# Performance work log

Hardware: AMD Instinct MI355X
Metric: run time of the kernel (lower is better)

Reference implementation:

```python
import jax, jax.numpy as jnp
import numpy as np

N_NODES = 100000
N_EDGES = 640000
IN_DIM = 64
HID = 128
NUM_GRAPHS = 128
MPNN_STEPS = 3
S2S_STEPS = 3


def setup_inputs() -> dict:
    key = jax.random.key(0)
    ks = jax.random.split(key, 20)
    x = jax.random.normal(ks[0], (N_NODES, IN_DIM), dtype=jnp.float32)
    edge_index = jax.random.randint(ks[1], (2, N_EDGES), 0, N_NODES, dtype=jnp.int32)
    batch = jnp.sort(jax.random.randint(ks[2], (N_NODES,), 0, NUM_GRAPHS, dtype=jnp.int32))
    s = 1.0 / np.sqrt(HID)
    params = {
        # input layer Linear(64 -> 128)
        'W_in': jax.random.normal(ks[3], (HID, IN_DIM), dtype=jnp.float32) * s,
        'b_in': jax.random.normal(ks[4], (HID,), dtype=jnp.float32) * s,
        # MGU parameters (torch.randn init in source)
        'W_f': jax.random.normal(ks[5], (HID, HID), dtype=jnp.float32),
        'U_f': jax.random.normal(ks[6], (HID, HID), dtype=jnp.float32),
        'b_f': jax.random.normal(ks[7], (HID,), dtype=jnp.float32),
        'W_h': jax.random.normal(ks[8], (HID, HID), dtype=jnp.float32),
        'U_h': jax.random.normal(ks[9], (HID, HID), dtype=jnp.float32),
        'b_h': jax.random.normal(ks[10], (HID,), dtype=jnp.float32),
        # Set2Set LSTM: input 2*HID, hidden HID, gate order i,f,g,o
        'lstm_w_ih': jax.random.normal(ks[11], (4 * HID, 2 * HID), dtype=jnp.float32) * s,
        'lstm_w_hh': jax.random.normal(ks[12], (4 * HID, HID), dtype=jnp.float32) * s,
        'lstm_b_ih': jax.random.normal(ks[13], (4 * HID,), dtype=jnp.float32) * s,
        'lstm_b_hh': jax.random.normal(ks[14], (4 * HID,), dtype=jnp.float32) * s,
        # prediction layer Linear(2*HID -> 1)
        'W_pred': jax.random.normal(ks[15], (1, 2 * HID), dtype=jnp.float32) * s,
        'b_pred': jax.random.normal(ks[16], (1,), dtype=jnp.float32) * s,
    }
    return {'x': x, 'edge_index': edge_index, 'batch': batch, **params}


def _mpnn_mgu(h, src, dst, W_f, U_f, b_f, W_h, U_h, b_h):
    # sum-aggregate neighbor messages: m_i = sum_{j->i} h_j
    m = jax.ops.segment_sum(h[src], dst, num_segments=N_NODES)  # [N, H]
    f_t = jax.nn.sigmoid(m @ W_f.T + h @ U_f.T + b_f)
    h_hat = jnp.tanh(m @ W_h.T + (f_t * h) @ U_h.T + b_h)
    return (1.0 - f_t) * h + f_t * h_hat


def _set2set(x, batch, w_ih, w_hh, b_ih, b_hh):
    G, H = NUM_GRAPHS, HID
    q_star = jnp.zeros((G, 2 * H), dtype=x.dtype)
    h_l = jnp.zeros((G, H), dtype=x.dtype)
    c_l = jnp.zeros((G, H), dtype=x.dtype)
    for _ in range(S2S_STEPS):
        gates = q_star @ w_ih.T + h_l @ w_hh.T + b_ih + b_hh  # [G, 4H]
        i, f, g, o = jnp.split(gates, 4, axis=-1)
        c_l = jax.nn.sigmoid(f) * c_l + jax.nn.sigmoid(i) * jnp.tanh(g)
        h_l = jax.nn.sigmoid(o) * jnp.tanh(c_l)
        q = h_l  # [G, H]
        # attention over nodes within each graph segment
        e = jnp.sum(x * q[batch], axis=-1)  # [N]
        e_max = jax.ops.segment_max(e, batch, num_segments=G)
        a_un = jnp.exp(e - e_max[batch])
        denom = jax.ops.segment_sum(a_un, batch, num_segments=G)
        a = a_un / denom[batch]
        r = jax.ops.segment_sum(a[:, None] * x, batch, num_segments=G)  # [G, H]
        q_star = jnp.concatenate([q, r], axis=-1)
    return q_star


def reference(x, edge_index, batch, W_in, b_in, W_f, U_f, b_f, W_h, U_h, b_h,
              lstm_w_ih, lstm_w_hh, lstm_b_ih, lstm_b_hh, W_pred, b_pred):
    h = jax.nn.relu(x @ W_in.T + b_in)  # [N, HID]
    src, dst = edge_index[0], edge_index[1]
    for _ in range(MPNN_STEPS):
        h = _mpnn_mgu(h, src, dst, W_f, U_f, b_f, W_h, U_h, b_h)
    q_star = _set2set(h, batch, lstm_w_ih, lstm_w_hh, lstm_b_ih, lstm_b_hh)  # [G, 2H]
    return q_star @ W_pred.T + b_pred  # [G, 1]
```

## Files before the change

### kernel.cpp

```cpp
#include <hip/hip_runtime.h>
#include <math.h>

#define N_NODES 100000
#define N_EDGES 640000
#define IN_DIM 64
#define HID 128
#define NGRAPH 128

typedef __bf16 bf16x2 __attribute__((ext_vector_type(2)));
typedef __bf16 bf16x4 __attribute__((ext_vector_type(4)));
typedef __bf16 bf16x8 __attribute__((ext_vector_type(8)));
typedef float f32x4 __attribute__((ext_vector_type(4)));

#define LDST 136

__device__ __forceinline__ float sigmoid_f(float z) {
  return __fdividef(1.f, 1.f + __expf(-z));
}
__device__ __forceinline__ float tanh_f(float z) {
  return 1.f - __fdividef(2.f, __expf(2.f * z) + 1.f);
}

__device__ __forceinline__ void fma44(const float4 A[4], const float4 B[4], float acc[4][4]) {
#pragma unroll
  for (int i2 = 0; i2 < 4; ++i2) {
    acc[i2][0] += A[i2].x*B[0].x + A[i2].y*B[1].x + A[i2].z*B[2].x + A[i2].w*B[3].x;
    acc[i2][1] += A[i2].x*B[0].y + A[i2].y*B[1].y + A[i2].z*B[2].y + A[i2].w*B[3].y;
    acc[i2][2] += A[i2].x*B[0].z + A[i2].y*B[1].z + A[i2].z*B[2].z + A[i2].w*B[3].z;
    acc[i2][3] += A[i2].x*B[0].w + A[i2].y*B[1].w + A[i2].z*B[2].w + A[i2].w*B[3].w;
  }
}

__global__ __launch_bounds__(256) void k_input(const float* __restrict__ x,
                                               const float* __restrict__ W,
                                               const float* __restrict__ b,
                                               float* __restrict__ h) {
  __shared__ float wS[64][132];
  __shared__ float xS[32][68];
  int t = threadIdx.x;
  int nb = blockIdx.x * 32;
#pragma unroll
  for (int i = 0; i < 8; ++i) {
    int idx4 = i * 256 + t;
    int j = idx4 >> 4, kq = idx4 & 15;
    float4 v = ((const float4*)W)[j * 16 + kq];
    wS[4*kq+0][j] = v.x; wS[4*kq+1][j] = v.y; wS[4*kq+2][j] = v.z; wS[4*kq+3][j] = v.w;
  }
#pragma unroll
  for (int i = 0; i < 2; ++i) {
    int idx4 = i * 256 + t;
    int n = idx4 >> 4, kq = idx4 & 15;
    float4 v = ((const float4*)x)[(nb + n) * 16 + kq];
    *((float4*)&xS[n][4*kq]) = v;
  }
  __syncthreads();
  int bq = t & 31, a = t >> 5;
  float acc[4][4] = {};
#pragma unroll
  for (int kk4 = 0; kk4 < 16; ++kk4) {
    float4 A[4], B[4];
#pragma unroll
    for (int i2 = 0; i2 < 4; ++i2) A[i2] = *((const float4*)&xS[4*a+i2][4*kk4]);
#pragma unroll
    for (int c = 0; c < 4; ++c) B[c] = *((const float4*)&wS[4*kk4+c][4*bq]);
    fma44(A, B, acc);
  }
  float4 bb = ((const float4*)b)[bq];
  float ba[4] = {bb.x, bb.y, bb.z, bb.w};
#pragma unroll
  for (int i2 = 0; i2 < 4; ++i2) {
    float4 o;
    o.x = fmaxf(acc[i2][0] + ba[0], 0.f);
    o.y = fmaxf(acc[i2][1] + ba[1], 0.f);
    o.z = fmaxf(acc[i2][2] + ba[2], 0.f);
    o.w = fmaxf(acc[i2][3] + ba[3], 0.f);
    ((float4*)h)[(nb + 4*a + i2) * 32 + bq] = o;
  }
}

__global__ __launch_bounds__(256) void k_hist(const int* __restrict__ dst,
                                              int* __restrict__ deg) {
  int e = blockIdx.x * 256 + threadIdx.x;
  if (e < N_EDGES) atomicAdd(&deg[dst[e]], 1);
}

#define SCAN_CHUNK 4096
#define SCAN_NB 25

__global__ __launch_bounds__(256) void k_scan_part(const int* __restrict__ deg,
                                                   int* __restrict__ bsum) {
  __shared__ int red[256];
  int t = threadIdx.x, b = blockIdx.x;
  int base = b * SCAN_CHUNK + t * 16;
  int s = 0;
#pragma unroll
  for (int i = 0; i < 16; ++i) {
    int idx = base + i;
    if (idx < N_NODES) s += deg[idx];
  }
  red[t] = s;
  __syncthreads();
  for (int off = 128; off > 0; off >>= 1) {
    if (t < off) red[t] += red[t + off];
    __syncthreads();
  }
  if (t == 0) bsum[b] = red[0];
}

__global__ void k_scan_mid(const int* __restrict__ bsum, int* __restrict__ boff,
                           int* __restrict__ rowstart) {
  if (threadIdx.x == 0) {
    int run = 0;
    for (int i = 0; i < SCAN_NB; ++i) { boff[i] = run; run += bsum[i]; }
    rowstart[N_NODES] = run;
  }
}

__global__ __launch_bounds__(256) void k_scan_final(const int* __restrict__ deg,
                                                    const int* __restrict__ boff,
                                                    int* __restrict__ rowstart) {
  __shared__ int ts[256];
  int t = threadIdx.x, b = blockIdx.x;
  int base = b * SCAN_CHUNK + t * 16;
  int v[16];
  int s = 0;
#pragma unroll
  for (int i = 0; i < 16; ++i) {
    int idx = base + i;
    v[i] = (idx < N_NODES) ? deg[idx] : 0;
    s += v[i];
  }
  ts[t] = s;
  __syncthreads();
  for (int off = 1; off < 256; off <<= 1) {
    int add = (t >= off) ? ts[t - off] : 0;
    __syncthreads();
    ts[t] += add;
    __syncthreads();
  }
  int run = boff[b] + ts[t] - s;
#pragma unroll
  for (int i = 0; i < 16; ++i) {
    int idx = base + i;
    if (idx < N_NODES) rowstart[idx] = run;
    run += v[i];
  }
}

__global__ __launch_bounds__(256) void k_fill(const int* __restrict__ src,
                                              const int* __restrict__ dst,
                                              int* __restrict__ cursor,
                                              int* __restrict__ srcSorted) {
  int e = blockIdx.x * 256 + threadIdx.x;
  if (e >= N_EDGES) return;
  int d = dst[e];
  int p = atomicAdd(&cursor[d], 1);
  srcSorted[p] = src[e];
}

__global__ __launch_bounds__(256) void k_wsplit(const float* __restrict__ W0,
                                                const float* __restrict__ W1,
                                                const float* __restrict__ W2,
                                                const float* __restrict__ W3,
                                                __bf16* __restrict__ Whi,
                                                __bf16* __restrict__ Wlo) {
  int id = blockIdx.x * 256 + threadIdx.x;
  int mat = id >> 14, idx = id & 16383;
  const float* W = (mat == 0) ? W0 : (mat == 1) ? W1 : (mat == 2) ? W2 : W3;
  float v = W[idx];
  __bf16 hi = (__bf16)v;
  Whi[id] = hi;
  Wlo[id] = (__bf16)(v - (float)hi);
}

__global__ __launch_bounds__(256, 4) void k_mgu(float* __restrict__ hdst,
                                                const float* __restrict__ hsrc,
                                                const int* __restrict__ rowstart,
                                                const int* __restrict__ srcSorted,
                                                const __bf16* __restrict__ Whi,
                                                const __bf16* __restrict__ Wlo,
                                                const float* __restrict__ bfp,
                                                const float* __restrict__ bhp) {
  __shared__ __bf16 mHi[32 * LDST], mLo[32 * LDST];
  __shared__ __bf16 hHi[32 * LDST], hLo[32 * LDST];
  const int t = threadIdx.x;
  const int nb = blockIdx.x * 32;

#pragma unroll
  for (int i = 0; i < 4; ++i) {
    int idx4 = i * 256 + t;
    int n = idx4 >> 5, kq = idx4 & 31;
    float4 vh = ((const float4*)hsrc)[(nb + n) * 32 + kq];
    bf16x4 hh, hl;
    hh[0] = (__bf16)vh.x; hl[0] = (__bf16)(vh.x - (float)hh[0]);
    hh[1] = (__bf16)vh.y; hl[1] = (__bf16)(vh.y - (float)hh[1]);
    hh[2] = (__bf16)vh.z; hl[2] = (__bf16)(vh.z - (float)hh[2]);
    hh[3] = (__bf16)vh.w; hl[3] = (__bf16)(vh.w - (float)hh[3]);
    int e0 = n * LDST + 4 * kq;
    *(bf16x4*)&hHi[e0] = hh; *(bf16x4*)&hLo[e0] = hl;
  }

  {
    const int grp = t >> 5, li = t & 31;
    const float4* h4 = (const float4*)hsrc;
#pragma unroll
    for (int c = 0; c < 4; ++c) {
      int nl = c * 8 + grp;
      int node = nb + nl;
      int j0 = rowstart[node], j1 = rowstart[node + 1];
      float4 a0 = {0.f, 0.f, 0.f, 0.f}, a1 = {0.f, 0.f, 0.f, 0.f};
      float4 a2 = {0.f, 0.f, 0.f, 0.f}, a3 = {0.f, 0.f, 0.f, 0.f};
      int j = j0;
      for (; j + 3 < j1; j += 4) {
        int s0 = srcSorted[j], s1 = srcSorted[j + 1];
        int s2 = srcSorted[j + 2], s3 = srcSorted[j + 3];
        float4 v0 = h4[s0 * 32 + li];
        float4 v1 = h4[s1 * 32 + li];
        float4 v2 = h4[s2 * 32 + li];
        float4 v3 = h4[s3 * 32 + li];
        a0.x += v0.x; a0.y += v0.y; a0.z += v0.z; a0.w += v0.w;
        a1.x += v1.x; a1.y += v1.y; a1.z += v1.z; a1.w += v1.w;
        a2.x += v2.x; a2.y += v2.y; a2.z += v2.z; a2.w += v2.w;
        a3.x += v3.x; a3.y += v3.y; a3.z += v3.z; a3.w += v3.w;
      }
      if (j + 1 < j1) {
        int s0 = srcSorted[j], s1 = srcSorted[j + 1];
        float4 v0 = h4[s0 * 32 + li];
        float4 v1 = h4[s1 * 32 + li];
        a0.x += v0.x; a0.y += v0.y; a0.z += v0.z; a0.w += v0.w;
        a1.x += v1.x; a1.y += v1.y; a1.z += v1.z; a1.w += v1.w;
        j += 2;
      }
      if (j < j1) {
        int s0 = srcSorted[j];
        float4 v0 = h4[s0 * 32 + li];
        a0.x += v0.x; a0.y += v0.y; a0.z += v0.z; a0.w += v0.w;
      }
      float4 o = {a0.x + a1.x + a2.x + a3.x, a0.y + a1.y + a2.y + a3.y,
                  a0.z + a1.z + a2.z + a3.z, a0.w + a1.w + a2.w + a3.w};
      bf16x4 mh, ml;
      mh[0] = (__bf16)o.x; ml[0] = (__bf16)(o.x - (float)mh[0]);
      mh[1] = (__bf16)o.y; ml[1] = (__bf16)(o.y - (float)mh[1]);
      mh[2] = (__bf16)o.z; ml[2] = (__bf16)(o.z - (float)mh[2]);
      mh[3] = (__bf16)o.w; ml[3] = (__bf16)(o.w - (float)mh[3]);
      int e0 = nl * LDST + 4 * li;
      *(bf16x4*)&mHi[e0] = mh; *(bf16x4*)&mLo[e0] = ml;
    }
  }
  __syncthreads();

  const int w = t >> 6, l = t & 63;
  const int lj = l & 15, q = l >> 4;

  float bfj[2], bhj[2];
#pragma unroll
  for (int ct = 0; ct < 2; ++ct) {
    int j = (2 * w + ct) * 16 + lj;
    bfj[ct] = bfp[j];
    bhj[ct] = bhp[j];
  }

  f32x4 acc[2][2] = {};

#pragma unroll
  for (int kc = 0; kc < 128; kc += 32) {
    bf16x8 bwh[2], bwl[2], buh[2], bul[2];
#pragma unroll
    for (int ct = 0; ct < 2; ++ct) {
      int off = ((2 * w + ct) * 16 + lj) * 128 + kc + q * 8;
      bwh[ct] = *(const bf16x8*)&Whi[off];
      bwl[ct] = *(const bf16x8*)&Wlo[off];
      buh[ct] = *(const bf16x8*)&Whi[16384 + off];
      bul[ct] = *(const bf16x8*)&Wlo[16384 + off];
    }
#pragma unroll
    for (int rt = 0; rt < 2; ++rt) {
      int e0 = (rt * 16 + lj) * LDST + kc + q * 8;
      bf16x8 amh = *(const bf16x8*)&mHi[e0];
      bf16x8 aml = *(const bf16x8*)&mLo[e0];
      bf16x8 ahh = *(const bf16x8*)&hHi[e0];
      bf16x8 ahl = *(const bf16x8*)&hLo[e0];
#pragma unroll
      for (int ct = 0; ct < 2; ++ct) {
        f32x4 a = acc[rt][ct];
        a = __builtin_amdgcn_mfma_f32_16x16x32_bf16(amh, bwh[ct], a, 0, 0, 0);
        a = __builtin_amdgcn_mfma_f32_16x16x32_bf16(amh, bwl[ct], a, 0, 0, 0);
        a = __builtin_amdgcn_mfma_f32_16x16x32_bf16(aml, bwh[ct], a, 0, 0, 0);
        a = __builtin_amdgcn_mfma_f32_16x16x32_bf16(ahh, buh[ct], a, 0, 0, 0);
        a = __builtin_amdgcn_mfma_f32_16x16x32_bf16(ahh, bul[ct], a, 0, 0, 0);
        a = __builtin_amdgcn_mfma_f32_16x16x32_bf16(ahl, buh[ct], a, 0, 0, 0);
        acc[rt][ct] = a;
      }
    }
  }

  __syncthreads();
  float fv[2][2][4], hvv[2][2][4];
#pragma unroll
  for (int rt = 0; rt < 2; ++rt)
#pragma unroll
    for (int ct = 0; ct < 2; ++ct) {
      int j = (2 * w + ct) * 16 + lj;
#pragma unroll
      for (int r = 0; r < 4; ++r) {
        int nl = rt * 16 + q * 4 + r;
        float z = acc[rt][ct][r] + bfj[ct];
        float f = sigmoid_f(z);
        int he = nl * LDST + j;
        float hval = (float)hHi[he] + (float)hLo[he];
        float g = f * hval;
        __bf16 ghi = (__bf16)g;
        hHi[he] = ghi;
        hLo[he] = (__bf16)(g - (float)ghi);
        fv[rt][ct][r] = f;
        hvv[rt][ct][r] = hval;
        acc[rt][ct][r] = 0.f;
      }
    }
  __syncthreads();

#pragma unroll
  for (int kc = 0; kc < 128; kc += 32) {
    bf16x8 bwh[2], bwl[2], buh[2], bul[2];
#pragma unroll
    for (int ct = 0; ct < 2; ++ct) {
      int off = ((2 * w + ct) * 16 + lj) * 128 + kc + q * 8;
      bwh[ct] = *(const bf16x8*)&Whi[2 * 16384 + off];
      bwl[ct] = *(const bf16x8*)&Wlo[2 * 16384 + off];
      buh[ct] = *(const bf16x8*)&Whi[3 * 16384 + off];
      bul[ct] = *(const bf16x8*)&Wlo[3 * 16384 + off];
    }
#pragma unroll
    for (int rt = 0; rt < 2; ++rt) {
      int e0 = (rt * 16 + lj) * LDST + kc + q * 8;
      bf16x8 amh = *(const bf16x8*)&mHi[e0];
      bf16x8 aml = *(const bf16x8*)&mLo[e0];
      bf16x8 agh = *(const bf16x8*)&hHi[e0];
      bf16x8 agl = *(const bf16x8*)&hLo[e0];
#pragma unroll
      for (int ct = 0; ct < 2; ++ct) {
        f32x4 a = acc[rt][ct];
        a = __builtin_amdgcn_mfma_f32_16x16x32_bf16(amh, bwh[ct], a, 0, 0, 0);
        a = __builtin_amdgcn_mfma_f32_16x16x32_bf16(amh, bwl[ct], a, 0, 0, 0);
        a = __builtin_amdgcn_mfma_f32_16x16x32_bf16(aml, bwh[ct], a, 0, 0, 0);
        a = __builtin_amdgcn_mfma_f32_16x16x32_bf16(agh, buh[ct], a, 0, 0, 0);
        a = __builtin_amdgcn_mfma_f32_16x16x32_bf16(agh, bul[ct], a, 0, 0, 0);
        a = __builtin_amdgcn_mfma_f32_16x16x32_bf16(agl, buh[ct], a, 0, 0, 0);
        acc[rt][ct] = a;
      }
    }
  }

#pragma unroll
  for (int rt = 0; rt < 2; ++rt)
#pragma unroll
    for (int ct = 0; ct < 2; ++ct) {
      int j = (2 * w + ct) * 16 + lj;
#pragma unroll
      for (int r = 0; r < 4; ++r) {
        int node = nb + rt * 16 + q * 4 + r;
        float T = tanh_f(acc[rt][ct][r] + bhj[ct]);
        float f = fv[rt][ct][r];
        float hn = (1.f - f) * hvv[rt][ct][r] + f * T;
        hdst[node * 128 + j] = hn;
      }
    }
}

__global__ __launch_bounds__(1024) void k_s2s(const float* __restrict__ h,
                                              const int* __restrict__ batch,
                                              const float* __restrict__ w_ih,
                                              const float* __restrict__ w_hh,
                                              const float* __restrict__ b_ih,
                                              const float* __restrict__ b_hh,
                                              const float* __restrict__ Wp,
                                              const float* __restrict__ bp,
                                              float* __restrict__ out) {
  const int g = blockIdx.x, t = threadIdx.x;
  const int w = t >> 6, l = t & 63;
  const int half = l >> 5, li = l & 31;
  const int hw = 2 * w + half;
  __shared__ float qs[256];
  __shared__ float hl[128], cl[128];
  __shared__ float gates[512];
  __shared__ float redM[32], redS[32], scl[32];
  __shared__ float rPart[32][132];
  __shared__ float gInvS;
  __shared__ int bnd[2];

  if (t < 2) {
    int tgt = g + t;
    int lo = 0, hi = N_NODES;
    while (lo < hi) { int mid = (lo + hi) >> 1; if (batch[mid] < tgt) lo = mid + 1; else hi = mid; }
    bnd[t] = lo;
  }
  if (t < 256) qs[t] = 0.f;
  if (t < 128) { hl[t] = 0.f; cl[t] = 0.f; }
  __syncthreads();
  const int s0 = bnd[0], s1 = bnd[1];

  for (int step = 0; step < 3; ++step) {
#pragma unroll 2
    for (int jt = w; jt < 512; jt += 16) {
      const float* wi = w_ih + jt * 256;
      const float* wh = w_hh + jt * 128;
      float s = qs[l] * wi[l] + qs[l+64] * wi[l+64]
              + qs[l+128] * wi[l+128] + qs[l+192] * wi[l+192]
              + hl[l] * wh[l] + hl[l+64] * wh[l+64];
#pragma unroll
      for (int o = 32; o > 0; o >>= 1) s += __shfl_xor(s, o, 64);
      if (l == 0) gates[jt] = s + b_ih[jt] + b_hh[jt];
    }
    __syncthreads();
    if (t < 128) {
      float gi = gates[t], gf = gates[128 + t], gg = gates[256 + t], go = gates[384 + t];
      float c = sigmoid_f(gf) * cl[t] + sigmoid_f(gi) * tanh_f(gg);
      float hh = sigmoid_f(go) * tanh_f(c);
      cl[t] = c;
      hl[t] = hh;
      qs[t] = hh;
    }
    __syncthreads();

    float mw = -INFINITY, sw = 0.f;
    float4 racc = {0.f, 0.f, 0.f, 0.f};
    const float4* h4 = (const float4*)h;
    const float q0 = qs[4*li], q1 = qs[4*li+1], q2 = qs[4*li+2], q3 = qs[4*li+3];
    int n = s0 + hw;
    for (; n + 32 < s1; n += 64) {
      float4 hv0 = h4[n * 32 + li];
      float4 hv1 = h4[(n + 32) * 32 + li];
      float v0 = hv0.x * q0 + hv0.y * q1 + hv0.z * q2 + hv0.w * q3;
      float v1 = hv1.x * q0 + hv1.y * q1 + hv1.z * q2 + hv1.w * q3;
#pragma unroll
      for (int o = 16; o > 0; o >>= 1) {
        v0 += __shfl_xor(v0, o, 64);
        v1 += __shfl_xor(v1, o, 64);
      }
      float nm = fmaxf(mw, fmaxf(v0, v1));
      float sc = __expf(mw - nm);
      float w0 = __expf(v0 - nm);
      float w1 = __expf(v1 - nm);
      sw = sw * sc + w0 + w1;
      racc.x = racc.x * sc + w0 * hv0.x + w1 * hv1.x;
      racc.y = racc.y * sc + w0 * hv0.y + w1 * hv1.y;
      racc.z = racc.z * sc + w0 * hv0.z + w1 * hv1.z;
      racc.w = racc.w * sc + w0 * hv0.w + w1 * hv1.w;
      mw = nm;
    }
    for (; n < s1; n += 32) {
      float4 hv = h4[n * 32 + li];
      float v = hv.x * q0 + hv.y * q1 + hv.z * q2 + hv.w * q3;
#pragma unroll
      for (int o = 16; o > 0; o >>= 1) v += __shfl_xor(v, o, 64);
      float nm = fmaxf(mw, v);
      float sc = __expf(mw - nm);
      float wg = __expf(v - nm);
      sw = sw * sc + wg;
      racc.x = racc.x * sc + wg * hv.x;
      racc.y = racc.y * sc + wg * hv.y;
      racc.z = racc.z * sc + wg * hv.z;
      racc.w = racc.w * sc + wg * hv.w;
      mw = nm;
    }
    if (li == 0) { redM[hw] = mw; redS[hw] = sw; }
    *(float4*)&rPart[hw][4 * li] = racc;
    __syncthreads();
    if (t == 0) {
      float M = -INFINITY;
      for (int i = 0; i < 32; ++i) M = fmaxf(M, redM[i]);
      float S = 0.f;
      for (int i = 0; i < 32; ++i) {
        float s_ = (redM[i] > -INFINITY && M > -INFINITY) ? __expf(redM[i] - M) : 0.f;
        scl[i] = s_;
        S += redS[i] * s_;
      }
      gInvS = (S > 0.f) ? __fdividef(1.f, S) : 0.f;
    }
    __syncthreads();
    if (t < 128) {
      float inv = gInvS;
      float r = 0.f;
#pragma unroll
      for (int i = 0; i < 32; ++i) r += rPart[i][t] * scl[i];
      qs[128 + t] = r * inv;
    }
    __syncthreads();
  }

  __shared__ float pr[256];
  if (t < 256) pr[t] = qs[t] * Wp[t];
  __syncthreads();
  if (t < 128) pr[t] += pr[t + 128];
  __syncthreads();
  if (t < 64) {
    float s = pr[t] + pr[t + 64];
#pragma unroll
    for (int o = 32; o > 0; o >>= 1) s += __shfl_xor(s, o, 64);
    if (t == 0) out[g] = s + bp[0];
  }
}

extern "C" void kernel_launch(void* const* d_in, const int* in_sizes, int n_in,
                              void* d_out, int out_size, void* d_ws, size_t ws_size,
                              hipStream_t stream) {
  const float* x      = (const float*)d_in[0];
  const int*   ei     = (const int*)d_in[1];
  const int*   batch  = (const int*)d_in[2];
  const float* W_in   = (const float*)d_in[3];
  const float* b_in   = (const float*)d_in[4];
  const float* W_f    = (const float*)d_in[5];
  const float* U_f    = (const float*)d_in[6];
  const float* b_f    = (const float*)d_in[7];
  const float* W_h    = (const float*)d_in[8];
  const float* U_h    = (const float*)d_in[9];
  const float* b_h    = (const float*)d_in[10];
  const float* w_ih   = (const float*)d_in[11];
  const float* w_hh   = (const float*)d_in[12];
  const float* b_ih   = (const float*)d_in[13];
  const float* b_hh   = (const float*)d_in[14];
  const float* W_pred = (const float*)d_in[15];
  const float* b_pred = (const float*)d_in[16];
  float* out = (float*)d_out;

  char* ws = (char*)d_ws;
  float* h0     = (float*)(ws);
  float* h1     = (float*)(ws + 51200000);
  int*   rowstart = (int*)(ws + 103063808);
  int*   srcSorted= (int*)(ws + 103463824);
  int*   bsum   = (int*)  (ws + 106023824);
  int*   boff   = (int*)  (ws + 106023936);
  int*    deg    = (int*)(ws + 102400000);
  int*    cursor = (int*)(ws + 102400000);
  __bf16* Whi    = (__bf16*)(ws + 102400000);
  __bf16* Wlo    = (__bf16*)(ws + 102531072);

  const int* src = ei;
  const int* dst = ei + N_EDGES;

  hipMemsetAsync(deg, 0, N_NODES * 4, stream);
  k_hist<<<(N_EDGES + 255) / 256, 256, 0, stream>>>(dst, deg);
  k_scan_part<<<SCAN_NB, 256, 0, stream>>>(deg, bsum);
  k_scan_mid<<<1, 32, 0, stream>>>(bsum, boff, rowstart);
  k_scan_final<<<SCAN_NB, 256, 0, stream>>>(deg, boff, rowstart);
  hipMemcpyAsync(cursor, rowstart, N_NODES * 4, hipMemcpyDeviceToDevice, stream);
  k_fill<<<(N_EDGES + 255) / 256, 256, 0, stream>>>(src, dst, cursor, srcSorted);

  k_wsplit<<<256, 256, 0, stream>>>(W_f, U_f, W_h, U_h, Whi, Wlo);

  k_input<<<N_NODES / 32, 256, 0, stream>>>(x, W_in, b_in, h0);

  const int NBLK = N_NODES / 32;
  k_mgu<<<NBLK, 256, 0, stream>>>(h1, h0, rowstart, srcSorted, Whi, Wlo, b_f, b_h);
  k_mgu<<<NBLK, 256, 0, stream>>>(h0, h1, rowstart, srcSorted, Whi, Wlo, b_f, b_h);
  k_mgu<<<NBLK, 256, 0, stream>>>(h1, h0, rowstart, srcSorted, Whi, Wlo, b_f, b_h);

  k_s2s<<<NGRAPH, 1024, 0, stream>>>(h1, batch, w_ih, w_hh, b_ih, b_hh,
                                     W_pred, b_pred, out);
}
```

Baseline: 747.0 us.

## Swizzle MGU shared tiles, raise occupancy, and batch 8 predicated neighbor gathers

Replaces the padded LDS row stride with an XOR swizzle, shrinking the shared tiles from 136 to 128 columns so a fifth block can fit per CU, and raises the launch-bound minimum occupancy to 5. The neighbor aggregation loop now issues 8 gathers per iteration with clamped indices and 0/1 weights instead of a 4-wide loop plus tails, aiming for more memory-level parallelism and fewer divergent branches. The outer node loop is left un-unrolled to hold register pressure down. In exchange, the clamped indices cause redundant loads of the last neighbor in partial batches, and the tighter register cap risks spills.

```diff
diff --git a/kernel.cpp b/kernel.cpp
--- a/kernel.cpp
+++ b/kernel.cpp
@@ -12,13 +12,21 @@
 typedef __bf16 bf16x8 __attribute__((ext_vector_type(8)));
 typedef float f32x4 __attribute__((ext_vector_type(4)));
 
-#define LDST 136
-
 __device__ __forceinline__ float sigmoid_f(float z) {
   return __fdividef(1.f, 1.f + __expf(-z));
 }
 __device__ __forceinline__ float tanh_f(float z) {
   return 1.f - __fdividef(2.f, __expf(2.f * z) + 1.f);
+}
+
+__device__ __forceinline__ int swz8(int row, int c8) {
+  return row * 128 + ((c8 ^ (row & 7)) << 3);
+}
+__device__ __forceinline__ int swz4(int row, int kq4) {
+  return row * 128 + ((((kq4 >> 1) ^ (row & 7)) << 3) + ((kq4 & 1) << 2));
+}
+__device__ __forceinline__ int swzE(int row, int col) {
+  return row * 128 + ((((col >> 3) ^ (row & 7)) << 3) + (col & 7));
 }
 
 __device__ __forceinline__ void fma44(const float4 A[4], const float4 B[4], float acc[4][4]) {
@@ -173,7 +181,7 @@
   Wlo[id] = (__bf16)(v - (float)hi);
 }
 
-__global__ __launch_bounds__(256, 4) void k_mgu(float* __restrict__ hdst,
+__global__ __launch_bounds__(256, 5) void k_mgu(float* __restrict__ hdst,
                                                 const float* __restrict__ hsrc,
                                                 const int* __restrict__ rowstart,
                                                 const int* __restrict__ srcSorted,
@@ -181,8 +189,8 @@
                                                 const __bf16* __restrict__ Wlo,
                                                 const float* __restrict__ bfp,
                                                 const float* __restrict__ bhp) {
-  __shared__ __bf16 mHi[32 * LDST], mLo[32 * LDST];
-  __shared__ __bf16 hHi[32 * LDST], hLo[32 * LDST];
+  __shared__ __bf16 mHi[32 * 128], mLo[32 * 128];
+  __shared__ __bf16 hHi[32 * 128], hLo[32 * 128];
   const int t = threadIdx.x;
   const int nb = blockIdx.x * 32;
 
@@ -196,54 +204,60 @@
     hh[1] = (__bf16)vh.y; hl[1] = (__bf16)(vh.y - (float)hh[1]);
     hh[2] = (__bf16)vh.z; hl[2] = (__bf16)(vh.z - (float)hh[2]);
     hh[3] = (__bf16)vh.w; hl[3] = (__bf16)(vh.w - (float)hh[3]);
-    int e0 = n * LDST + 4 * kq;
+    int e0 = swz4(n, kq);
     *(bf16x4*)&hHi[e0] = hh; *(bf16x4*)&hLo[e0] = hl;
   }
 
   {
     const int grp = t >> 5, li = t & 31;
     const float4* h4 = (const float4*)hsrc;
-#pragma unroll
+#pragma unroll 1
     for (int c = 0; c < 4; ++c) {
       int nl = c * 8 + grp;
       int node = nb + nl;
       int j0 = rowstart[node], j1 = rowstart[node + 1];
       float4 a0 = {0.f, 0.f, 0.f, 0.f}, a1 = {0.f, 0.f, 0.f, 0.f};
-      float4 a2 = {0.f, 0.f, 0.f, 0.f}, a3 = {0.f, 0.f, 0.f, 0.f};
-      int j = j0;
-      for (; j + 3 < j1; j += 4) {
-        int s0 = srcSorted[j], s1 = srcSorted[j + 1];
-        int s2 = srcSorted[j + 2], s3 = srcSorted[j + 3];
+      int jlast = j1 - 1;
+      for (int j = j0; j < j1; j += 8) {
+        int s0 = srcSorted[j];
+        int s1 = srcSorted[min(j + 1, jlast)];
+        int s2 = srcSorted[min(j + 2, jlast)];
+        int s3 = srcSorted[min(j + 3, jlast)];
+        int s4 = srcSorted[min(j + 4, jlast)];
+        int s5 = srcSorted[min(j + 5, jlast)];
+        int s6 = srcSorted[min(j + 6, jlast)];
+        int s7 = srcSorted[min(j + 7, jlast)];
         float4 v0 = h4[s0 * 32 + li];
         float4 v1 = h4[s1 * 32 + li];
         float4 v2 = h4[s2 * 32 + li];
         float4 v3 = h4[s3 * 32 + li];
-        a0.x += v0.x; a0.y += v0.y; a0.z += v0.z; a0.w += v0.w;
-        a1.x += v1.x; a1.y += v1.y; a1.z += v1.z; a1.w += v1.w;
-        a2.x += v2.x; a2.y += v2.y; a2.z += v2.z; a2.w += v2.w;
-        a3.x += v3.x; a3.y += v3.y; a3.z += v3.z; a3.w += v3.w;
-      }
-      if (j + 1 < j1) {
-        int s0 = srcSorted[j], s1 = srcSorted[j + 1];
-        float4 v0 = h4[s0 * 32 + li];
-        float4 v1 = h4[s1 * 32 + li];
-        a0.x += v0.x; a0.y += v0.y; a0.z += v0.z; a0.w += v0.w;
-        a1.x += v1.x; a1.y += v1.y; a1.z += v1.z; a1.w += v1.w;
-        j += 2;
-      }
-      if (j < j1) {
-        int s0 = srcSorted[j];
-        float4 v0 = h4[s0 * 32 + li];
-        a0.x += v0.x; a0.y += v0.y; a0.z += v0.z; a0.w += v0.w;
-      }
-      float4 o = {a0.x + a1.x + a2.x + a3.x, a0.y + a1.y + a2.y + a3.y,
-                  a0.z + a1.z + a2.z + a3.z, a0.w + a1.w + a2.w + a3.w};
+        float4 v4 = h4[s4 * 32 + li];
+        float4 v5 = h4[s5 * 32 + li];
+        float4 v6 = h4[s6 * 32 + li];
+        float4 v7 = h4[s7 * 32 + li];
+        float w1 = (j + 1 < j1) ? 1.f : 0.f;
+        float w2 = (j + 2 < j1) ? 1.f : 0.f;
+        float w3 = (j + 3 < j1) ? 1.f : 0.f;
+        float w4 = (j + 4 < j1) ? 1.f : 0.f;
+        float w5 = (j + 5 < j1) ? 1.f : 0.f;
+        float w6 = (j + 6 < j1) ? 1.f : 0.f;
+        float w7 = (j + 7 < j1) ? 1.f : 0.f;
+        a0.x += v0.x + w2 * v2.x; a0.y += v0.y + w2 * v2.y;
+        a0.z += v0.z + w2 * v2.z; a0.w += v0.w + w2 * v2.w;
+        a1.x += w1 * v1.x + w3 * v3.x; a1.y += w1 * v1.y + w3 * v3.y;
+        a1.z += w1 * v1.z + w3 * v3.z; a1.w += w1 * v1.w + w3 * v3.w;
+        a0.x += w4 * v4.x + w6 * v6.x; a0.y += w4 * v4.y + w6 * v6.y;
+        a0.z += w4 * v4.z + w6 * v6.z; a0.w += w4 * v4.w + w6 * v6.w;
+        a1.x += w5 * v5.x + w7 * v7.x; a1.y += w5 * v5.y + w7 * v7.y;
+        a1.z += w5 * v5.z + w7 * v7.z; a1.w += w5 * v5.w + w7 * v7.w;
+      }
+      float4 o = {a0.x + a1.x, a0.y + a1.y, a0.z + a1.z, a0.w + a1.w};
       bf16x4 mh, ml;
       mh[0] = (__bf16)o.x; ml[0] = (__bf16)(o.x - (float)mh[0]);
       mh[1] = (__bf16)o.y; ml[1] = (__bf16)(o.y - (float)mh[1]);
       mh[2] = (__bf16)o.z; ml[2] = (__bf16)(o.z - (float)mh[2]);
       mh[3] = (__bf16)o.w; ml[3] = (__bf16)(o.w - (float)mh[3]);
-      int e0 = nl * LDST + 4 * li;
+      int e0 = swz4(nl, li);
       *(bf16x4*)&mHi[e0] = mh; *(bf16x4*)&mLo[e0] = ml;
     }
   }
@@ -275,7 +289,7 @@
     }
 #pragma unroll
     for (int rt = 0; rt < 2; ++rt) {
-      int e0 = (rt * 16 + lj) * LDST + kc + q * 8;
+      int e0 = swz8(rt * 16 + lj, (kc >> 3) + q);
       bf16x8 amh = *(const bf16x8*)&mHi[e0];
       bf16x8 aml = *(const bf16x8*)&mLo[e0];
       bf16x8 ahh = *(const bf16x8*)&hHi[e0];
@@ -306,7 +320,7 @@
         int nl = rt * 16 + q * 4 + r;
         float z = acc[rt][ct][r] + bfj[ct];
         float f = sigmoid_f(z);
-        int he = nl * LDST + j;
+        int he = swzE(nl, j);
         float hval = (float)hHi[he] + (float)hLo[he];
         float g = f * hval;
         __bf16 ghi = (__bf16)g;
@@ -332,7 +346,7 @@
     }
 #pragma unroll
     for (int rt = 0; rt < 2; ++rt) {
-      int e0 = (rt * 16 + lj) * LDST + kc + q * 8;
+      int e0 = swz8(rt * 16 + lj, (kc >> 3) + q);
       bf16x8 amh = *(const bf16x8*)&mHi[e0];
       bf16x8 aml = *(const bf16x8*)&mLo[e0];
       bf16x8 agh = *(const bf16x8*)&hHi[e0];
```

Result: slower. 796.2 us (+6.6%).

## Split Set2Set attention scan across multiple blocks per graph with separate LSTM combine kernel

Applied to the files above, without the earlier changes.

Replaces the single per-graph Set2Set kernel with three kernels: an init kernel that computes the first LSTM step from biases, a scan kernel that splits each graph's nodes over four blocks producing partial softmax statistics, and a combine kernel that merges the partials and computes the next LSTM step. This raises block-level parallelism from one block per graph to four, so more CUs can work on the attention reduction. In exchange it adds several extra kernel launches per step, global round-trips for partials and state, and an LSTM gate matvec with strided per-thread weight reads.

```diff
diff --git a/kernel.cpp b/kernel.cpp
--- a/kernel.cpp
+++ b/kernel.cpp
@@ -6,6 +6,8 @@
 #define IN_DIM 64
 #define HID 128
 #define NGRAPH 128
+#define SPLIT 4
+#define PSTR 132
 
 typedef __bf16 bf16x2 __attribute__((ext_vector_type(2)));
 typedef __bf16 bf16x4 __attribute__((ext_vector_type(4)));
@@ -367,25 +369,35 @@
     }
 }
 
-__global__ __launch_bounds__(1024) void k_s2s(const float* __restrict__ h,
-                                              const int* __restrict__ batch,
-                                              const float* __restrict__ w_ih,
-                                              const float* __restrict__ w_hh,
-                                              const float* __restrict__ b_ih,
-                                              const float* __restrict__ b_hh,
-                                              const float* __restrict__ Wp,
-                                              const float* __restrict__ bp,
-                                              float* __restrict__ out) {
-  const int g = blockIdx.x, t = threadIdx.x;
+__global__ __launch_bounds__(128) void k_s2s_init(const float* __restrict__ b_ih,
+                                                  const float* __restrict__ b_hh,
+                                                  float* __restrict__ q_buf,
+                                                  float* __restrict__ hc_buf) {
+  int g = blockIdx.x, t = threadIdx.x;
+  float gi = b_ih[t] + b_hh[t];
+  float gf = b_ih[128 + t] + b_hh[128 + t];
+  float gg = b_ih[256 + t] + b_hh[256 + t];
+  float go = b_ih[384 + t] + b_hh[384 + t];
+  float c = sigmoid_f(gi) * tanh_f(gg);
+  float hh = sigmoid_f(go) * tanh_f(c);
+  q_buf[g * 128 + t] = hh;
+  hc_buf[g * 256 + t] = hh;
+  hc_buf[g * 256 + 128 + t] = c;
+}
+
+__global__ __launch_bounds__(1024, 8) void k_s2s_scan(const float* __restrict__ h,
+                                                      const int* __restrict__ batch,
+                                                      const float* __restrict__ q_buf,
+                                                      float* __restrict__ partials) {
+  const int b = blockIdx.x;
+  const int g = b >> 2, p = b & (SPLIT - 1);
+  const int t = threadIdx.x;
   const int w = t >> 6, l = t & 63;
   const int half = l >> 5, li = l & 31;
   const int hw = 2 * w + half;
-  __shared__ float qs[256];
-  __shared__ float hl[128], cl[128];
-  __shared__ float gates[512];
   __shared__ float redM[32], redS[32], scl[32];
   __shared__ float rPart[32][132];
-  __shared__ float gInvS;
+  __shared__ float sMS[2];
   __shared__ int bnd[2];
 
   if (t < 2) {
@@ -394,110 +406,170 @@
     while (lo < hi) { int mid = (lo + hi) >> 1; if (batch[mid] < tgt) lo = mid + 1; else hi = mid; }
     bnd[t] = lo;
   }
-  if (t < 256) qs[t] = 0.f;
-  if (t < 128) { hl[t] = 0.f; cl[t] = 0.f; }
   __syncthreads();
   const int s0 = bnd[0], s1 = bnd[1];
-
-  for (int step = 0; step < 3; ++step) {
-#pragma unroll 2
-    for (int jt = w; jt < 512; jt += 16) {
-      const float* wi = w_ih + jt * 256;
-      const float* wh = w_hh + jt * 128;
-      float s = qs[l] * wi[l] + qs[l+64] * wi[l+64]
-              + qs[l+128] * wi[l+128] + qs[l+192] * wi[l+192]
-              + hl[l] * wh[l] + hl[l+64] * wh[l+64];
+  const int len = s1 - s0;
+  const int ps = s0 + (len * p) / SPLIT;
+  const int pe = s0 + (len * (p + 1)) / SPLIT;
+
+  float4 qv = ((const float4*)(q_buf + g * 128))[li];
+  const float q0 = qv.x, q1 = qv.y, q2 = qv.z, q3 = qv.w;
+
+  float mw = -INFINITY, sw = 0.f;
+  float4 racc = {0.f, 0.f, 0.f, 0.f};
+  const float4* h4 = (const float4*)h;
+  int n = ps + hw;
+  for (; n + 32 < pe; n += 64) {
+    float4 hv0 = h4[n * 32 + li];
+    float4 hv1 = h4[(n + 32) * 32 + li];
+    float v0 = hv0.x * q0 + hv0.y * q1 + hv0.z * q2 + hv0.w * q3;
+    float v1 = hv1.x * q0 + hv1.y * q1 + hv1.z * q2 + hv1.w * q3;
+#pragma unroll
+    for (int o = 16; o > 0; o >>= 1) {
+      v0 += __shfl_xor(v0, o, 64);
+      v1 += __shfl_xor(v1, o, 64);
+    }
+    float nm = fmaxf(mw, fmaxf(v0, v1));
+    float sc = __expf(mw - nm);
+    float w0 = __expf(v0 - nm);
+    float w1 = __expf(v1 - nm);
+    sw = sw * sc + w0 + w1;
+    racc.x = racc.x * sc + w0 * hv0.x + w1 * hv1.x;
+    racc.y = racc.y * sc + w0 * hv0.y + w1 * hv1.y;
+    racc.z = racc.z * sc + w0 * hv0.z + w1 * hv1.z;
+    racc.w = racc.w * sc + w0 * hv0.w + w1 * hv1.w;
+    mw = nm;
+  }
+  for (; n < pe; n += 32) {
+    float4 hv = h4[n * 32 + li];
+    float v = hv.x * q0 + hv.y * q1 + hv.z * q2 + hv.w * q3;
+#pragma unroll
+    for (int o = 16; o > 0; o >>= 1) v += __shfl_xor(v, o, 64);
+    float nm = fmaxf(mw, v);
+    float sc = __expf(mw - nm);
+    float wg = __expf(v - nm);
+    sw = sw * sc + wg;
+    racc.x = racc.x * sc + wg * hv.x;
+    racc.y = racc.y * sc + wg * hv.y;
+    racc.z = racc.z * sc + wg * hv.z;
+    racc.w = racc.w * sc + wg * hv.w;
+    mw = nm;
+  }
+  if (li == 0) { redM[hw] = mw; redS[hw] = sw; }
+  *(float4*)&rPart[hw][4 * li] = racc;
+  __syncthreads();
+  if (t == 0) {
+    float M = -INFINITY;
+    for (int i = 0; i < 32; ++i) M = fmaxf(M, redM[i]);
+    float S = 0.f;
+    for (int i = 0; i < 32; ++i) {
+      float s_ = (redM[i] > -INFINITY && M > -INFINITY) ? __expf(redM[i] - M) : 0.f;
+      scl[i] = s_;
+      S += redS[i] * s_;
+    }
+    sMS[0] = M; sMS[1] = S;
+  }
+  __syncthreads();
+  float* P = partials + (g * SPLIT + p) * PSTR;
+  if (t == 0) { P[0] = sMS[0]; P[1] = sMS[1]; }
+  if (t < 128) {
+    float r = 0.f;
+#pragma unroll
+    for (int i = 0; i < 32; ++i) r += rPart[i][t] * scl[i];
+    P[4 + t] = r;
+  }
+}
+
+__global__ __launch_bounds__(256) void k_s2s_combine(float* __restrict__ q_buf,
+                                                     float* __restrict__ hc_buf,
+                                                     const float* __restrict__ partials,
+                                                     const float* __restrict__ w_ih,
+                                                     const float* __restrict__ w_hh,
+                                                     const float* __restrict__ b_ih,
+                                                     const float* __restrict__ b_hh,
+                                                     const float* __restrict__ Wp,
+                                                     const float* __restrict__ bp,
+                                                     float* __restrict__ out,
+                                                     int last) {
+  const int g = blockIdx.x, t = threadIdx.x;
+  __shared__ float sc[SPLIT];
+  __shared__ float qstar[256];
+  __shared__ float hcl[256];
+  __shared__ float gates[512];
+  __shared__ float invS_sh;
+  const float* P = partials + g * SPLIT * PSTR;
+
+  if (t == 0) {
+    float M = -INFINITY;
+#pragma unroll
+    for (int p = 0; p < SPLIT; ++p) M = fmaxf(M, P[p * PSTR]);
+    float S = 0.f;
+#pragma unroll
+    for (int p = 0; p < SPLIT; ++p) {
+      float mp = P[p * PSTR];
+      float s_ = (mp > -INFINITY && M > -INFINITY) ? __expf(mp - M) : 0.f;
+      sc[p] = s_;
+      S += P[p * PSTR + 1] * s_;
+    }
+    invS_sh = (S > 0.f) ? __fdividef(1.f, S) : 0.f;
+  }
+  if (t < 128) {
+    qstar[t] = q_buf[g * 128 + t];
+    hcl[t] = hc_buf[g * 256 + t];
+    hcl[128 + t] = hc_buf[g * 256 + 128 + t];
+  }
+  __syncthreads();
+  if (t < 128) {
+    float r = 0.f;
+#pragma unroll
+    for (int p = 0; p < SPLIT; ++p) r += P[p * PSTR + 4 + t] * sc[p];
+    qstar[128 + t] = r * invS_sh;
+  }
+  __syncthreads();
+
+  if (last) {
+    __shared__ float pr[256];
+    pr[t] = qstar[t] * Wp[t];
+    __syncthreads();
+    if (t < 128) pr[t] += pr[t + 128];
+    __syncthreads();
+    if (t < 64) {
+      float s = pr[t] + pr[t + 64];
 #pragma unroll
       for (int o = 32; o > 0; o >>= 1) s += __shfl_xor(s, o, 64);
-      if (l == 0) gates[jt] = s + b_ih[jt] + b_hh[jt];
-    }
-    __syncthreads();
-    if (t < 128) {
-      float gi = gates[t], gf = gates[128 + t], gg = gates[256 + t], go = gates[384 + t];
-      float c = sigmoid_f(gf) * cl[t] + sigmoid_f(gi) * tanh_f(gg);
-      float hh = sigmoid_f(go) * tanh_f(c);
-      cl[t] = c;
-      hl[t] = hh;
-      qs[t] = hh;
-    }
-    __syncthreads();
-
-    float mw = -INFINITY, sw = 0.f;
-    float4 racc = {0.f, 0.f, 0.f, 0.f};
-    const float4* h4 = (const float4*)h;
-    const float q0 = qs[4*li], q1 = qs[4*li+1], q2 = qs[4*li+2], q3 = qs[4*li+3];
-    int n = s0 + hw;
-    for (; n + 32 < s1; n += 64) {
-      float4 hv0 = h4[n * 32 + li];
-      float4 hv1 = h4[(n + 32) * 32 + li];
-      float v0 = hv0.x * q0 + hv0.y * q1 + hv0.z * q2 + hv0.w * q3;
-      float v1 = hv1.x * q0 + hv1.y * q1 + hv1.z * q2 + hv1.w * q3;
-#pragma unroll
-      for (int o = 16; o > 0; o >>= 1) {
-        v0 += __shfl_xor(v0, o, 64);
-        v1 += __shfl_xor(v1, o, 64);
-      }
-      float nm = fmaxf(mw, fmaxf(v0, v1));
-      float sc = __expf(mw - nm);
-      float w0 = __expf(v0 - nm);
-      float w1 = __expf(v1 - nm);
-      sw = sw * sc + w0 + w1;
-      racc.x = racc.x * sc + w0 * hv0.x + w1 * hv1.x;
-      racc.y = racc.y * sc + w0 * hv0.y + w1 * hv1.y;
-      racc.z = racc.z * sc + w0 * hv0.z + w1 * hv1.z;
-      racc.w = racc.w * sc + w0 * hv0.w + w1 * hv1.w;
-      mw = nm;
-    }
-    for (; n < s1; n += 32) {
-      float4 hv = h4[n * 32 + li];
-      float v = hv.x * q0 + hv.y * q1 + hv.z * q2 + hv.w * q3;
-#pragma unroll
-      for (int o = 16; o > 0; o >>= 1) v += __shfl_xor(v, o, 64);
-      float nm = fmaxf(mw, v);
-      float sc = __expf(mw - nm);
-      float wg = __expf(v - nm);
-      sw = sw * sc + wg;
-      racc.x = racc.x * sc + wg * hv.x;
-      racc.y = racc.y * sc + wg * hv.y;
-      racc.z = racc.z * sc + wg * hv.z;
-      racc.w = racc.w * sc + wg * hv.w;
-      mw = nm;
-    }
-    if (li == 0) { redM[hw] = mw; redS[hw] = sw; }
-    *(float4*)&rPart[hw][4 * li] = racc;
-    __syncthreads();
-    if (t == 0) {
-      float M = -INFINITY;
-      for (int i = 0; i < 32; ++i) M = fmaxf(M, redM[i]);
-      float S = 0.f;
-      for (int i = 0; i < 32; ++i) {
-        float s_ = (redM[i] > -INFINITY && M > -INFINITY) ? __expf(redM[i] - M) : 0.f;
-        scl[i] = s_;
-        S += redS[i] * s_;
-      }
-      gInvS = (S > 0.f) ? __fdividef(1.f, S) : 0.f;
-    }
-    __syncthreads();
-    if (t < 128) {
-      float inv = gInvS;
-      float r = 0.f;
-#pragma unroll
-      for (int i = 0; i < 32; ++i) r += rPart[i][t] * scl[i];
-      qs[128 + t] = r * inv;
-    }
-    __syncthreads();
-  }
-
-  __shared__ float pr[256];
-  if (t < 256) pr[t] = qs[t] * Wp[t];
-  __syncthreads();
-  if (t < 128) pr[t] += pr[t + 128];
-  __syncthreads();
-  if (t < 64) {
-    float s = pr[t] + pr[t + 64];
-#pragma unroll
-    for (int o = 32; o > 0; o >>= 1) s += __shfl_xor(s, o, 64);
-    if (t == 0) out[g] = s + bp[0];
+      if (t == 0) out[g] = s + bp[0];
+    }
+    return;
+  }
+
+#pragma unroll
+  for (int rr = 0; rr < 2; ++rr) {
+    int j = t + rr * 256;
+    const float4* wi4 = (const float4*)(w_ih + j * 256);
+    const float4* wh4 = (const float4*)(w_hh + j * 128);
+    float s = 0.f;
+#pragma unroll 8
+    for (int k = 0; k < 64; ++k) {
+      float4 a = wi4[k];
+      float4 b = *(const float4*)&qstar[4 * k];
+      s += a.x * b.x + a.y * b.y + a.z * b.z + a.w * b.w;
+    }
+#pragma unroll 8
+    for (int k = 0; k < 32; ++k) {
+      float4 a = wh4[k];
+      float4 b = *(const float4*)&hcl[4 * k];
+      s += a.x * b.x + a.y * b.y + a.z * b.z + a.w * b.w;
+    }
+    gates[j] = s + b_ih[j] + b_hh[j];
+  }
+  __syncthreads();
+  if (t < 128) {
+    float gi = gates[t], gf = gates[128 + t], gg = gates[256 + t], go = gates[384 + t];
+    float c = sigmoid_f(gf) * hcl[128 + t] + sigmoid_f(gi) * tanh_f(gg);
+    float hh = sigmoid_f(go) * tanh_f(c);
+    hc_buf[g * 256 + t] = hh;
+    hc_buf[g * 256 + 128 + t] = c;
+    q_buf[g * 128 + t] = hh;
   }
 }
 
@@ -534,6 +606,9 @@
   int*    cursor = (int*)(ws + 102400000);
   __bf16* Whi    = (__bf16*)(ws + 102400000);
   __bf16* Wlo    = (__bf16*)(ws + 102531072);
+  float* q_buf    = (float*)(ws);
+  float* hc_buf   = (float*)(ws + 65536);
+  float* partials = (float*)(ws + 196608);
 
   const int* src = ei;
   const int* dst = ei + N_EDGES;
@@ -555,6 +630,11 @@
   k_mgu<<<NBLK, 256, 0, stream>>>(h0, h1, rowstart, srcSorted, Whi, Wlo, b_f, b_h);
   k_mgu<<<NBLK, 256, 0, stream>>>(h1, h0, rowstart, srcSorted, Whi, Wlo, b_f, b_h);
 
-  k_s2s<<<NGRAPH, 1024, 0, stream>>>(h1, batch, w_ih, w_hh, b_ih, b_hh,
-                                     W_pred, b_pred, out);
-}
+  k_s2s_init<<<NGRAPH, 128, 0, stream>>>(b_ih, b_hh, q_buf, hc_buf);
+  for (int step = 0; step < 3; ++step) {
+    k_s2s_scan<<<NGRAPH * SPLIT, 1024, 0, stream>>>(h1, batch, q_buf, partials);
+    k_s2s_combine<<<NGRAPH, 256, 0, stream>>>(q_buf, hc_buf, partials,
+                                              w_ih, w_hh, b_ih, b_hh,
+                                              W_pred, b_pred, out, step == 2);
+  }
+}
```

Result: no change. 752.9 us (+0.8%).
